# Performance work log

Hardware: AMD Instinct MI355X
Metric: run time of the kernel (lower is better)

## Reference

```python
import jax, jax.numpy as jnp
import numpy as np

B, H, W, C = 16, 64, 64, 256
NH = 8          # num_heads
WS = 8          # window size (8,8) from shift=2
HID = 1024      # mlp hidden = 4*C
EPS = 1e-5


def _rel_index():
    # relative_position_index exactly as in the torch module (meshgrid 'ij')
    ch = np.arange(WS)
    coords = np.stack(np.meshgrid(ch, ch, indexing='ij'))          # (2, WS, WS)
    flat = coords.reshape(2, -1)                                    # (2, N)
    rel = flat[:, :, None] - flat[:, None, :]                       # (2, N, N)
    rel = rel.transpose(1, 2, 0).astype(np.int64)                   # (N, N, 2)
    rel[..., 0] += WS - 1
    rel[..., 1] += WS - 1
    rel[..., 0] *= 2 * WS - 1
    return jnp.asarray(rel.sum(-1))                                 # (N, N)


def _ln(x, w, b):
    m = x.mean(-1, keepdims=True)
    v = jnp.mean((x - m) ** 2, axis=-1, keepdims=True)
    return (x - m) / jnp.sqrt(v + EPS) * w + b


def setup_inputs() -> dict:
    key = jax.random.key(0)
    ks = jax.random.split(key, 16)
    std = 0.02
    n_bias = (2 * WS - 1) * (2 * WS - 1)  # 225
    return {
        'x': jax.random.normal(ks[0], (B, H * W, C), jnp.float32),
        'norm1_w': jnp.ones((C,), jnp.float32),
        'norm1_b': jnp.zeros((C,), jnp.float32),
        'qkv_w': jax.random.normal(ks[1], (3 * C, C), jnp.float32) * std,
        'qkv_b': jnp.zeros((3 * C,), jnp.float32),
        'rel_bias': jax.random.normal(ks[2], (n_bias, NH), jnp.float32) * std,
        'proj_w': jax.random.normal(ks[3], (C, C), jnp.float32) * std,
        'proj_b': jnp.zeros((C,), jnp.float32),
        'norm2_w': jnp.ones((C,), jnp.float32),
        'norm2_b': jnp.zeros((C,), jnp.float32),
        'fc1_w': jax.random.normal(ks[4], (HID, C), jnp.float32) * std,
        'fc1_b': jnp.zeros((HID,), jnp.float32),
        'dw_w': jax.random.normal(ks[5], (3, 3, 1, HID), jnp.float32) * std,  # HWIO depthwise
        'dw_b': jnp.zeros((HID,), jnp.float32),
        'fc2_w': jax.random.normal(ks[6], (C, HID), jnp.float32) * std,
        'fc2_b': jnp.zeros((C,), jnp.float32),
    }


def reference(x, norm1_w, norm1_b, qkv_w, qkv_b, rel_bias, proj_w, proj_b,
              norm2_w, norm2_b, fc1_w, fc1_b, dw_w, dw_b, fc2_w, fc2_b):
    S = (H // WS) * (W // WS)   # num windows = 64
    N = WS * WS                 # tokens per window = 64
    shortcut = x
    h = _ln(x, norm1_w, norm1_b).reshape(B, H, W, C)
    # window partition -> (B, S, N, C), then permute to (B, N, S, C)
    hw = (h.reshape(B, H // WS, WS, W // WS, WS, C)
            .transpose(0, 1, 3, 2, 4, 5)
            .reshape(B, S, N, C))
    xw = hw.transpose(0, 2, 1, 3)            # (B, N, S, C)
    # qkv over flattened (N*S) tokens; heads split the S*C feature dim
    xf = xw.reshape(B, N * S, C)
    qkv = xf @ qkv_w.T + qkv_b               # (B, N*S, 3C)
    qkv = qkv.reshape(B, N, 3, NH, S * C // NH).transpose(2, 0, 3, 1, 4)
    q, k, v = qkv[0], qkv[1], qkv[2]         # (B, NH, N, S*C/NH)
    scale = (C // NH) ** -0.5
    attn = jnp.einsum('bhnd,bhmd->bhnm', q, k) * scale   # (B, NH, N, N)
    idx = _rel_index()
    bias = rel_bias[idx.reshape(-1)].reshape(N, N, NH).transpose(2, 0, 1)
    attn = jax.nn.softmax(attn + bias[None], axis=-1)
    out = jnp.einsum('bhnm,bhmd->bhnd', attn, v)         # (B, NH, N, S*C/NH)
    out = out.transpose(0, 2, 1, 3).reshape(B, N * S, C)
    out = (out @ proj_w.T + proj_b).reshape(B, N, S, C).transpose(0, 2, 1, 3)  # (B,S,N,C)
    # window reverse -> (B, H*W, C)
    xr = (out.reshape(B, H // WS, W // WS, WS, WS, C)
             .transpose(0, 1, 3, 2, 4, 5)
             .reshape(B, H * W, C))
    x = shortcut + xr
    # conv-based MLP (eval mode, dropout = identity)
    y = _ln(x, norm2_w, norm2_b).reshape(B, H, H, C)      # NHWC
    y = jnp.einsum('bhwc,oc->bhwo', y, fc1_w) + fc1_b     # 1x1 conv
    y = jax.lax.conv_general_dilated(
        y, dw_w, (1, 1), 'SAME',
        dimension_numbers=('NHWC', 'HWIO', 'NHWC'),
        feature_group_count=HID) + dw_b
    y = jax.nn.gelu(y, approximate=False)
    y = jnp.einsum('bhwo,co->bhwc', y, fc2_w) + fc2_b     # 1x1 conv
    return x + y.reshape(B, H * W, C)
```

## Files before the change

### kernel.cpp

```cpp
#include <hip/hip_runtime.h>
#include <hip/hip_bf16.h>
#include <cstdint>
#include <cstddef>

#define B_     16
#define HW_    4096
#define C_     256
#define NH_    8
#define S_     64
#define N_     64
#define C3_    768
#define HID_   1024
#define DHEAD_ 2048
#define EPS_   1e-5f

using u16 = unsigned short;
using u32 = unsigned int;

typedef __attribute__((ext_vector_type(8))) short bf16x8;
typedef __attribute__((ext_vector_type(4))) float f32x4;

__device__ __forceinline__ float bf2f(u16 u) {
  union { float f; u32 i; } x; x.i = ((u32)u) << 16; return x.f;
}
__device__ __forceinline__ u16 f2bf(float f) {
  union { float f; u32 i; } x; x.f = f;
  u32 r = (x.i + 0x7FFFu + ((x.i >> 16) & 1u)) >> 16;
  return (u16)r;
}

__device__ __forceinline__ void gload_lds16(const u16* g, u16* l) {
  __builtin_amdgcn_global_load_lds(
      (const __attribute__((address_space(1))) unsigned int*)g,
      (__attribute__((address_space(3))) unsigned int*)l, 16, 0, 0);
}

__launch_bounds__(256)
__global__ void pack_w_kernel(const float* __restrict__ W, u16* __restrict__ out,
                              int K, int kshift) {
  int g = blockIdx.x * 256 + threadIdx.x;
  int lane = g & 63;
  int pk = g >> 6;
  int cb = pk >> kshift;
  int kb = pk & ((1 << kshift) - 1);
  int j = cb * 16 + (lane & 15);
  int k = kb * 32 + ((lane >> 4) << 3);
  const float* src = W + (size_t)j * K + k;
  float4 a = ((const float4*)src)[0];
  float4 b = ((const float4*)src)[1];
  ushort4 lo = {f2bf(a.x), f2bf(a.y), f2bf(a.z), f2bf(a.w)};
  ushort4 hi = {f2bf(b.x), f2bf(b.y), f2bf(b.z), f2bf(b.w)};
  ushort4* dst = (ushort4*)(out + (size_t)g * 8);
  dst[0] = lo;
  dst[1] = hi;
}

__launch_bounds__(256)
__global__ void ln_kernel(const float* __restrict__ in, const float* __restrict__ w,
                          const float* __restrict__ bias, u16* __restrict__ out,
                          int b_base) {
  int wave = threadIdx.x >> 6;
  int lane = threadIdx.x & 63;
  int t = blockIdx.x * 4 + wave;
  int b = b_base + (t >> 12);
  int r = t & 4095;
  int n = r >> 6, s = r & 63;
  int hw = (((s >> 3) << 3) + (n >> 3)) * 64 + ((s & 7) << 3) + (n & 7);
  size_t src_row = ((size_t)b << 12) + hw;
  float4 v = ((const float4*)(in + src_row * C_))[lane];
  float sum = v.x + v.y + v.z + v.w;
#pragma unroll
  for (int off = 32; off; off >>= 1) sum += __shfl_xor(sum, off);
  float mean = sum * (1.0f / C_);
  float4 d = {v.x - mean, v.y - mean, v.z - mean, v.w - mean};
  float ss = d.x * d.x + d.y * d.y + d.z * d.z + d.w * d.w;
#pragma unroll
  for (int off = 32; off; off >>= 1) ss += __shfl_xor(ss, off);
  float rstd = rsqrtf(ss * (1.0f / C_) + EPS_);
  float4 w4 = ((const float4*)w)[lane];
  float4 b4 = ((const float4*)bias)[lane];
  ushort4 o;
  o.x = f2bf(d.x * rstd * w4.x + b4.x);
  o.y = f2bf(d.y * rstd * w4.y + b4.y);
  o.z = f2bf(d.z * rstd * w4.z + b4.z);
  o.w = f2bf(d.w * rstd * w4.w + b4.w);
  ((ushort4*)(out + (size_t)t * C_))[lane] = o;
}

template<int K_, int J_, int EPI>
__launch_bounds__(256)
__global__ void gemm_mfma(const u16* __restrict__ A, const u16* __restrict__ wpk,
                          const float* __restrict__ bias, u16* __restrict__ outB,
                          float* __restrict__ outF, const float* __restrict__ res,
                          int m_base, u16* __restrict__ qb, u16* __restrict__ kb,
                          u16* __restrict__ vt) {
  constexpr int NT = K_ / 64;
  __shared__ u16 As[2][128 * 64];
  int tid = threadIdx.x;
  int wid = tid >> 6, lane = tid & 63;
  int nx = gridDim.x;
  int bid = blockIdx.y * nx + blockIdx.x;
  int cpx = (nx * gridDim.y) >> 3;
  int swz = (bid & 7) * cpx + (bid >> 3);
  int n0 = (swz % nx) * 128;
  int m0 = (swz / nx) * 128;
  int wr = wid >> 1, wc = wid & 1;
  f32x4 acc[4][4] = {};
  int srow8 = lane >> 3, sslot = lane & 7;

#define ASTAGE(buf, t)                                                         \
  {                                                                            \
    int k0g = (t) * 64;                                                        \
    int cbb = ((sslot ^ srow8) << 4);                                          \
    _Pragma("unroll")                                                          \
    for (int r = 0; r < 4; ++r) {                                              \
      int row = wid * 32 + r * 8 + srow8;                                      \
      gload_lds16(A + (size_t)(m0 + row) * K_ + k0g + (cbb >> 1),              \
                  &As[buf][(wid * 32 + r * 8) * 64]);                          \
    }                                                                          \
  }

  ASTAGE(0, 0);
  asm volatile("s_waitcnt vmcnt(0)" ::: "memory");
  __builtin_amdgcn_sched_barrier(0);
  __builtin_amdgcn_s_barrier();
  __builtin_amdgcn_sched_barrier(0);

  for (int t = 0; t < NT; ++t) {
    bf16x8 bfr[8];
#pragma unroll
    for (int kk = 0; kk < 2; ++kk)
#pragma unroll
      for (int nf = 0; nf < 4; ++nf)
        bfr[kk * 4 + nf] = *(const bf16x8*)&wpk[
            ((size_t)(((n0 >> 4) + wc * 4 + nf) * (K_ / 32) + (t * 2 + kk)) * 64 + lane) * 8];
    if (t + 1 < NT) ASTAGE((t + 1) & 1, t + 1);
    const u16* as = As[t & 1];
#pragma unroll
    for (int kk = 0; kk < 2; ++kk) {
      bf16x8 afr[4];
#pragma unroll
      for (int mf = 0; mf < 4; ++mf) {
        int ra = wr * 64 + mf * 16 + (lane & 15);
        int cbb = (((kk * 4 + (lane >> 4)) ^ (ra & 7)) << 4);
        afr[mf] = *(const bf16x8*)&as[ra * 64 + (cbb >> 1)];
      }
#pragma unroll
      for (int mf = 0; mf < 4; ++mf)
#pragma unroll
        for (int nf = 0; nf < 4; ++nf)
          acc[mf][nf] = __builtin_amdgcn_mfma_f32_16x16x32_bf16(afr[mf], bfr[kk * 4 + nf], acc[mf][nf], 0, 0, 0);
    }
    asm volatile("s_waitcnt vmcnt(0)" ::: "memory");
    __builtin_amdgcn_sched_barrier(0);
    __builtin_amdgcn_s_barrier();
    __builtin_amdgcn_sched_barrier(0);
  }
#undef ASTAGE

#pragma unroll
  for (int nf = 0; nf < 4; ++nf) {
    int col = n0 + wc * 64 + nf * 16 + (lane & 15);
    float bv = bias[col];
#pragma unroll
    for (int mf = 0; mf < 4; ++mf) {
#pragma unroll
      for (int j = 0; j < 4; ++j) {
        int m = m0 + wr * 64 + mf * 16 + (lane >> 4) * 4 + j;
        float v = acc[mf][nf][j] + bv;
        if (EPI == 0) {
          outB[(size_t)m * J_ + col] = f2bf(v);
        } else if (EPI == 2) {
          size_t o = (size_t)(m_base + m) * C_ + col;
          outF[o] += v;
        } else {
          int b_rel = m >> 12, nn = (m >> 6) & 63, s = m & 63;
          int f = s * 768 + col;
          int part = f >> 14, hh = (f >> 11) & 7, d = f & 2047;
          u16 val = f2bf(v);
          size_t bh = (size_t)b_rel * 8 + hh;
          if (part == 0)      qb[(bh * 64 + nn) * 2048 + d] = val;
          else if (part == 1) kb[(bh * 64 + nn) * 2048 + d] = val;
          else                vt[(bh * 2048 + d) * 64 + nn] = val;
        }
      }
    }
  }
}

__launch_bounds__(256)
__global__ void proj_ln_fused(const u16* __restrict__ A, const u16* __restrict__ wpk,
                              const float* __restrict__ bias, const float* __restrict__ res,
                              float* __restrict__ outF, const float* __restrict__ ln_w,
                              const float* __restrict__ ln_b, u16* __restrict__ h2,
                              int m_base) {
  __shared__ u16 As[2][64 * 64];
  __shared__ float red[64][8];
  int tid = threadIdx.x;
  int wid = tid >> 6, lane = tid & 63;
  int m0 = blockIdx.x * 64;
  f32x4 acc[4][4] = {};
  int srow8 = lane >> 3, sslot = lane & 7;

#define PSTAGE(buf, t)                                                         \
  {                                                                            \
    int k0g = (t) * 64;                                                        \
    int cbb = ((sslot ^ srow8) << 4);                                          \
    _Pragma("unroll")                                                          \
    for (int r = 0; r < 2; ++r) {                                              \
      int row = wid * 16 + r * 8 + srow8;                                      \
      gload_lds16(A + (size_t)(m0 + row) * 256 + k0g + (cbb >> 1),             \
                  &As[buf][(wid * 16 + r * 8) * 64]);                          \
    }                                                                          \
  }

  PSTAGE(0, 0);
  asm volatile("s_waitcnt vmcnt(0)" ::: "memory");
  __builtin_amdgcn_sched_barrier(0);
  __builtin_amdgcn_s_barrier();
  __builtin_amdgcn_sched_barrier(0);

#pragma unroll
  for (int t = 0; t < 4; ++t) {
    bf16x8 bfr[8];
#pragma unroll
    for (int kk = 0; kk < 2; ++kk)
#pragma unroll
      for (int nf = 0; nf < 4; ++nf)
        bfr[kk * 4 + nf] = *(const bf16x8*)&wpk[
            ((size_t)((wid * 4 + nf) * 8 + (t * 2 + kk)) * 64 + lane) * 8];
    if (t + 1 < 4) PSTAGE((t + 1) & 1, t + 1);
    const u16* as = As[t & 1];
#pragma unroll
    for (int kk = 0; kk < 2; ++kk) {
      bf16x8 afr[4];
#pragma unroll
      for (int mf = 0; mf < 4; ++mf) {
        int ra = mf * 16 + (lane & 15);
        int cbb = (((kk * 4 + (lane >> 4)) ^ (ra & 7)) << 4);
        afr[mf] = *(const bf16x8*)&as[ra * 64 + (cbb >> 1)];
      }
#pragma unroll
      for (int mf = 0; mf < 4; ++mf)
#pragma unroll
        for (int nf = 0; nf < 4; ++nf)
          acc[mf][nf] = __builtin_amdgcn_mfma_f32_16x16x32_bf16(afr[mf], bfr[kk * 4 + nf], acc[mf][nf], 0, 0, 0);
    }
    asm volatile("s_waitcnt vmcnt(0)" ::: "memory");
    __builtin_amdgcn_sched_barrier(0);
    __builtin_amdgcn_s_barrier();
    __builtin_amdgcn_sched_barrier(0);
  }
#undef PSTAGE

#pragma unroll
  for (int mf = 0; mf < 4; ++mf) {
#pragma unroll
    for (int j = 0; j < 4; ++j) {
      int m = m0 + mf * 16 + (lane >> 4) * 4 + j;
      int gm = m_base + m;
      int b = gm >> 12, nn = (gm >> 6) & 63, s = gm & 63;
      int hw = (((s >> 3) << 3) + (nn >> 3)) * 64 + ((s & 7) << 3) + (nn & 7);
      size_t rowo = (((size_t)b << 12) + hw) * C_;
      float s1 = 0.f, s2 = 0.f;
#pragma unroll
      for (int nf = 0; nf < 4; ++nf) {
        int col = wid * 64 + nf * 16 + (lane & 15);
        float v = acc[mf][nf][j] + bias[col] + res[rowo + col];
        acc[mf][nf][j] = v;
        outF[rowo + col] = v;
        s1 += v; s2 += v * v;
      }
#pragma unroll
      for (int off = 1; off < 16; off <<= 1) {
        s1 += __shfl_xor(s1, off);
        s2 += __shfl_xor(s2, off);
      }
      if ((lane & 15) == 0) {
        int rr = mf * 16 + (lane >> 4) * 4 + j;
        red[rr][wid * 2] = s1;
        red[rr][wid * 2 + 1] = s2;
      }
    }
  }
  __syncthreads();

#pragma unroll
  for (int mf = 0; mf < 4; ++mf) {
#pragma unroll
    for (int j = 0; j < 4; ++j) {
      int rr = mf * 16 + (lane >> 4) * 4 + j;
      float sum = red[rr][0] + red[rr][2] + red[rr][4] + red[rr][6];
      float ssq = red[rr][1] + red[rr][3] + red[rr][5] + red[rr][7];
      float mean = sum * (1.0f / C_);
      float var = ssq * (1.0f / C_) - mean * mean;
      float rstd = rsqrtf(var + EPS_);
      int m = m0 + rr;
      int b_rel = m >> 12, nn = (m >> 6) & 63, s = m & 63;
      int hw = (((s >> 3) << 3) + (nn >> 3)) * 64 + ((s & 7) << 3) + (nn & 7);
      size_t ho = (((size_t)b_rel << 12) + hw) * C_;
#pragma unroll
      for (int nf = 0; nf < 4; ++nf) {
        int col = wid * 64 + nf * 16 + (lane & 15);
        float nv = (acc[mf][nf][j] - mean) * rstd * ln_w[col] + ln_b[col];
        h2[ho + col] = f2bf(nv);
      }
    }
  }
}

__launch_bounds__(256)
__global__ void attn_mfma(const u16* __restrict__ qb, const u16* __restrict__ kb,
                          const u16* __restrict__ vt, const float* __restrict__ rel_bias,
                          u16* __restrict__ outp) {
  __shared__ u16 bufA[4096];
  __shared__ u16 bufB[4096];
  int bid = blockIdx.x;
  int half = bid & 1;
  int bh = bid >> 1;
  int h = bh & 7;
  int b_rel = bh >> 3;
  int tid = threadIdx.x;
  int w = tid >> 6, lane = tid & 63;
  int l3 = lane >> 3, l7 = lane & 7;
  const u16* qg = qb + (size_t)bh * 64 * 2048;
  const u16* kg = kb + (size_t)bh * 64 * 2048;
  const u16* vg = vt + (size_t)bh * 2048 * 64;

  f32x4 acc[4] = {};
  for (int k0 = 0; k0 < 2048; k0 += 64) {
#pragma unroll
    for (int r = 0; r < 2; ++r) {
      int row = w * 16 + r * 8 + l3;
      int sc = (l7 ^ (row & 7)) * 8;
      gload_lds16(qg + (size_t)row * 2048 + k0 + sc, &bufA[(w * 16 + r * 8) * 64]);
      gload_lds16(kg + (size_t)row * 2048 + k0 + sc, &bufB[(w * 16 + r * 8) * 64]);
    }
    __syncthreads();
    int rowq = w * 16 + (lane & 15);
#pragma unroll
    for (int ks = 0; ks < 2; ++ks) {
      bf16x8 aq = *(const bf16x8*)&bufA[rowq * 64 + (((ks * 4 + (lane >> 4)) ^ (rowq & 7)) << 3)];
#pragma unroll
      for (int cf = 0; cf < 4; ++cf) {
        int m = cf * 16 + (lane & 15);
        bf16x8 bk = *(const bf16x8*)&bufB[m * 64 + (((ks * 4 + (lane >> 4)) ^ (m & 7)) << 3)];
        acc[cf] = __builtin_amdgcn_mfma_f32_16x16x32_bf16(aq, bk, acc[cf], 0, 0, 0);
      }
    }
    __syncthreads();
  }

  const float scale = 0.17677669529663688f;
#pragma unroll
  for (int j = 0; j < 4; ++j) {
    int r = w * 16 + (lane >> 4) * 4 + j;
    int i1 = r >> 3, j1 = r & 7;
    float v[4];
#pragma unroll
    for (int cf = 0; cf < 4; ++cf) {
      int c = cf * 16 + (lane & 15);
      int idx = (i1 - (c >> 3) + 7) * 15 + (j1 - (c & 7) + 7);
      v[cf] = acc[cf][j] * scale + rel_bias[idx * NH_ + h];
    }
    float mx = fmaxf(fmaxf(v[0], v[1]), fmaxf(v[2], v[3]));
#pragma unroll
    for (int off = 8; off; off >>= 1) mx = fmaxf(mx, __shfl_xor(mx, off));
    float sm = 0.f;
#pragma unroll
    for (int cf = 0; cf < 4; ++cf) { v[cf] = __expf(v[cf] - mx); sm += v[cf]; }
#pragma unroll
    for (int off = 8; off; off >>= 1) sm += __shfl_xor(sm, off);
    float inv = 1.0f / sm;
#pragma unroll
    for (int cf = 0; cf < 4; ++cf) {
      int c = cf * 16 + (lane & 15);
      bufA[r * 64 + (c ^ ((r & 7) << 3))] = f2bf(v[cf] * inv);
    }
  }
  __syncthreads();

  bf16x8 pa[2];
  {
    int n = w * 16 + (lane & 15);
#pragma unroll
    for (int ks = 0; ks < 2; ++ks)
      pa[ks] = *(const bf16x8*)&bufA[n * 64 + ((ks * 32 + (lane >> 4) * 8) ^ ((n & 7) << 3))];
  }

  int d0beg = half * 1024;
  for (int d0 = d0beg; d0 < d0beg + 1024; d0 += 64) {
#pragma unroll
    for (int r = 0; r < 2; ++r) {
      int drow = w * 16 + r * 8 + l3;
      int sc = (l7 ^ (drow & 7)) * 8;
      gload_lds16(vg + (size_t)(d0 + drow) * 64 + sc, &bufB[(w * 16 + r * 8) * 64]);
    }
    __syncthreads();
    f32x4 o[4] = {};
#pragma unroll
    for (int ks = 0; ks < 2; ++ks)
#pragma unroll
      for (int cf = 0; cf < 4; ++cf) {
        int d = cf * 16 + (lane & 15);
        bf16x8 bv = *(const bf16x8*)&bufB[d * 64 + (((ks * 4 + (lane >> 4)) ^ (d & 7)) << 3)];
        o[cf] = __builtin_amdgcn_mfma_f32_16x16x32_bf16(pa[ks], bv, o[cf], 0, 0, 0);
      }
#pragma unroll
    for (int cf = 0; cf < 4; ++cf) {
      int f = h * 2048 + d0 + cf * 16 + (lane & 15);
      int s = f >> 8, c = f & 255;
#pragma unroll
      for (int j = 0; j < 4; ++j) {
        int n = w * 16 + (lane >> 4) * 4 + j;
        outp[(((size_t)b_rel * 64 + n) * 64 + s) * 256 + c] = f2bf(o[cf][j]);
      }
    }
    __syncthreads();
  }
}

__launch_bounds__(256)
__global__ void dwconv_gelu(const u16* __restrict__ y1, const float* __restrict__ dw_w,
                            const float* __restrict__ dw_b, u16* __restrict__ y2) {
  int bid = blockIdx.x;
  int wt = bid & 31, ht = (bid >> 5) & 15, b = bid >> 9;
  int h0 = ht * 4, w0 = wt * 2;
  int c0 = threadIdx.x * 4;

  float4 wv[9];
#pragma unroll
  for (int i = 0; i < 9; ++i) wv[i] = *(const float4*)&dw_w[i * HID_ + c0];

  ushort4 in[6][4];
#pragma unroll
  for (int ii = 0; ii < 6; ++ii) {
    int hh = h0 + ii - 1;
#pragma unroll
    for (int jj = 0; jj < 4; ++jj) {
      int ww = w0 + jj - 1;
      if ((unsigned)hh < 64u && (unsigned)ww < 64u)
        in[ii][jj] = *(const ushort4*)(y1 + ((size_t)((b << 12) + hh * 64 + ww)) * HID_ + c0);
      else
        in[ii][jj] = ushort4{0, 0, 0, 0};
    }
  }

  float4 bv = *(const float4*)&dw_b[c0];
  float4 acc[4][2];
#pragma unroll
  for (int i = 0; i < 4; ++i)
#pragma unroll
    for (int j = 0; j < 2; ++j) acc[i][j] = bv;

#pragma unroll
  for (int ii = 0; ii < 6; ++ii) {
#pragma unroll
    for (int jj = 0; jj < 4; ++jj) {
      ushort4 u = in[ii][jj];
      float4 f = {bf2f(u.x), bf2f(u.y), bf2f(u.z), bf2f(u.w)};
#pragma unroll
      for (int kh = 0; kh < 3; ++kh) {
        int i = ii - kh;
        if (i < 0 || i > 3) continue;
#pragma unroll
        for (int kw = 0; kw < 3; ++kw) {
          int j = jj - kw;
          if (j < 0 || j > 1) continue;
          float4 w4 = wv[kh * 3 + kw];
          acc[i][j].x += f.x * w4.x;
          acc[i][j].y += f.y * w4.y;
          acc[i][j].z += f.z * w4.z;
          acc[i][j].w += f.w * w4.w;
        }
      }
    }
  }

  const float k = 0.70710678118654752f;
#pragma unroll
  for (int i = 0; i < 4; ++i) {
#pragma unroll
    for (int j = 0; j < 2; ++j) {
      float4 a = acc[i][j];
      ushort4 o;
      o.x = f2bf(0.5f * a.x * (1.0f + erff(a.x * k)));
      o.y = f2bf(0.5f * a.y * (1.0f + erff(a.y * k)));
      o.z = f2bf(0.5f * a.z * (1.0f + erff(a.z * k)));
      o.w = f2bf(0.5f * a.w * (1.0f + erff(a.w * k)));
      *(ushort4*)(y2 + ((size_t)((b << 12) + (h0 + i) * 64 + (w0 + j))) * HID_ + c0) = o;
    }
  }
}

extern "C" void kernel_launch(void* const* d_in, const int* in_sizes, int n_in,
                              void* d_out, int out_size, void* d_ws, size_t ws_size,
                              hipStream_t stream) {
  const float* x       = (const float*)d_in[0];
  const float* norm1_w = (const float*)d_in[1];
  const float* norm1_b = (const float*)d_in[2];
  const float* qkv_w   = (const float*)d_in[3];
  const float* qkv_b   = (const float*)d_in[4];
  const float* rel_b   = (const float*)d_in[5];
  const float* proj_w  = (const float*)d_in[6];
  const float* proj_b  = (const float*)d_in[7];
  const float* norm2_w = (const float*)d_in[8];
  const float* norm2_b = (const float*)d_in[9];
  const float* fc1_w   = (const float*)d_in[10];
  const float* fc1_b   = (const float*)d_in[11];
  const float* dw_w    = (const float*)d_in[12];
  const float* dw_b    = (const float*)d_in[13];
  const float* fc2_w   = (const float*)d_in[14];
  const float* fc2_b   = (const float*)d_in[15];
  float* out = (float*)d_out;
  char* ws = (char*)d_ws;

  u16* wq = (u16*)(ws);
  u16* wp = wq + 768 * 256;
  u16* w1 = wp + 256 * 256;
  u16* w2 = w1 + 1024 * 256;
  pack_w_kernel<<<768 * 256 / 8 / 256, 256, 0, stream>>>(qkv_w, wq, 256, 3);
  pack_w_kernel<<<256 * 256 / 8 / 256, 256, 0, stream>>>(proj_w, wp, 256, 3);
  pack_w_kernel<<<1024 * 256 / 8 / 256, 256, 0, stream>>>(fc1_w, w1, 256, 3);
  pack_w_kernel<<<256 * 1024 / 8 / 256, 256, 0, stream>>>(fc2_w, w2, 1024, 5);

  const size_t MBy = (size_t)1 << 20;
  char* cws = ws + 2 * MBy;
  int G = 1;
  for (int g = 16; g >= 1; g >>= 1) {
    if (2 * MBy + (size_t)(18 * g) * MBy <= ws_size) { G = g; break; }
  }
  const size_t gm = (size_t)G * MBy;
  u16* h1c    = (u16*)(cws);
  u16* qbuf   = (u16*)(cws + 2 * gm);
  u16* kbuf   = (u16*)(cws + 4 * gm);
  u16* vtbuf  = (u16*)(cws + 6 * gm);
  u16* attnoc = (u16*)(cws + 8 * gm);
  u16* h2c    = (u16*)(cws);
  u16* y1c    = (u16*)(cws + 2 * gm);
  u16* y2c    = (u16*)(cws + 10 * gm);

  const int Mloc = G * 4096;
  for (int b0 = 0; b0 < B_; b0 += G) {
    ln_kernel<<<Mloc / 4, 256, 0, stream>>>(x, norm1_w, norm1_b, h1c, b0);
    gemm_mfma<256, 768, 3><<<dim3(6, Mloc / 128), 256, 0, stream>>>(
        h1c, wq, qkv_b, nullptr, nullptr, nullptr, 0, qbuf, kbuf, vtbuf);
    attn_mfma<<<G * 16, 256, 0, stream>>>(qbuf, kbuf, vtbuf, rel_b, attnoc);
    proj_ln_fused<<<Mloc / 64, 256, 0, stream>>>(
        attnoc, wp, proj_b, x, out, norm2_w, norm2_b, h2c, b0 * 4096);
    gemm_mfma<256, 1024, 0><<<dim3(8, Mloc / 128), 256, 0, stream>>>(
        h2c, w1, fc1_b, y1c, nullptr, nullptr, 0, nullptr, nullptr, nullptr);
    dwconv_gelu<<<Mloc / 8, 256, 0, stream>>>(y1c, dw_w, dw_b, y2c);
    gemm_mfma<1024, 256, 2><<<dim3(2, Mloc / 128), 256, 0, stream>>>(
        y2c, w2, fc2_b, nullptr, out, nullptr, b0 * 4096, nullptr, nullptr, nullptr);
  }
}
```

Before: 477.2 us.

## Stage GEMM epilogues through LDS and remap block indices for XCD locality

The GEMM epilogues for the bf16 output and fp32 residual-accumulate paths now write accumulator tiles into shared memory first, then emit row-contiguous 16-byte vector stores and float4 read-modify-writes. This replaces the scattered 2-byte and 4-byte per-lane global accesses. The attention and depthwise-conv kernels also remap blockIdx so that consecutive logical blocks land on the same XCD, which aims to improve L2 reuse on the chiplet layout. The cost is extra LDS traffic and barriers in the epilogue. The remap assumes the grid size is divisible by 8.

Result: no change. 481.3 us (+0.9%).

```diff
diff --git a/kernel.cpp b/kernel.cpp
--- a/kernel.cpp
+++ b/kernel.cpp
@@ -158,22 +158,77 @@
   }
 #undef ASTAGE
 
-#pragma unroll
-  for (int nf = 0; nf < 4; ++nf) {
-    int col = n0 + wc * 64 + nf * 16 + (lane & 15);
-    float bv = bias[col];
-#pragma unroll
-    for (int mf = 0; mf < 4; ++mf) {
-#pragma unroll
-      for (int j = 0; j < 4; ++j) {
-        int m = m0 + wr * 64 + mf * 16 + (lane >> 4) * 4 + j;
-        float v = acc[mf][nf][j] + bv;
-        if (EPI == 0) {
-          outB[(size_t)m * J_ + col] = f2bf(v);
-        } else if (EPI == 2) {
-          size_t o = (size_t)(m_base + m) * C_ + col;
-          outF[o] += v;
-        } else {
+  if (EPI == 0) {
+    u16* ot = (u16*)As;
+#pragma unroll
+    for (int half = 0; half < 2; ++half) {
+      if (wr == half) {
+#pragma unroll
+        for (int nf = 0; nf < 4; ++nf) {
+          int cloc = wc * 64 + nf * 16 + (lane & 15);
+          float bv = bias[n0 + cloc];
+#pragma unroll
+          for (int mf = 0; mf < 4; ++mf)
+#pragma unroll
+            for (int j = 0; j < 4; ++j) {
+              int rloc = mf * 16 + (lane >> 4) * 4 + j;
+              ot[rloc * 136 + cloc] = f2bf(acc[mf][nf][j] + bv);
+            }
+        }
+      }
+      __syncthreads();
+#pragma unroll
+      for (int i = 0; i < 4; ++i) {
+        int c = tid + 256 * i;
+        int row = c >> 4, ch = c & 15;
+        bf16x8 v = *(const bf16x8*)&ot[row * 136 + ch * 8];
+        *(bf16x8*)&outB[(size_t)(m0 + half * 64 + row) * J_ + n0 + ch * 8] = v;
+      }
+      __syncthreads();
+    }
+  } else if (EPI == 2) {
+    float* ot32 = (float*)As;
+#pragma unroll
+    for (int q = 0; q < 4; ++q) {
+      if (wr == (q >> 1)) {
+        int mfb = (q & 1) * 2;
+#pragma unroll
+        for (int nf = 0; nf < 4; ++nf) {
+          int cloc = wc * 64 + nf * 16 + (lane & 15);
+          float bv = bias[n0 + cloc];
+#pragma unroll
+          for (int mf2 = 0; mf2 < 2; ++mf2)
+#pragma unroll
+            for (int j = 0; j < 4; ++j) {
+              int rloc = mf2 * 16 + (lane >> 4) * 4 + j;
+              ot32[rloc * 132 + cloc] = acc[mfb + mf2][nf][j] + bv;
+            }
+        }
+      }
+      __syncthreads();
+#pragma unroll
+      for (int i = 0; i < 4; ++i) {
+        int c = tid + 256 * i;
+        int row = c >> 5, ch = c & 31;
+        size_t o = (size_t)(m_base + m0 + q * 32 + row) * C_ + n0 + ch * 4;
+        float4 cur = *(const float4*)&outF[o];
+        float4 ad = *(const float4*)&ot32[row * 132 + ch * 4];
+        cur.x += ad.x; cur.y += ad.y; cur.z += ad.z; cur.w += ad.w;
+        *(float4*)&outF[o] = cur;
+      }
+      __syncthreads();
+    }
+  } else {
+#pragma unroll
+    for (int nf = 0; nf < 4; ++nf) {
+      int col = n0 + wc * 64 + nf * 16 + (lane & 15);
+      float bv = bias[col];
+#pragma unroll
+      for (int mf = 0; mf < 4; ++mf) {
+#pragma unroll
+        for (int j = 0; j < 4; ++j) {
+          int m = m0 + wr * 64 + mf * 16 + (lane >> 4) * 4 + j;
+          float v = acc[mf][nf][j] + bv;
           int b_rel = m >> 12, nn = (m >> 6) & 63, s = m & 63;
           int f = s * 768 + col;
           int part = f >> 14, hh = (f >> 11) & 7, d = f & 2047;
@@ -315,9 +370,11 @@
                           u16* __restrict__ outp) {
   __shared__ u16 bufA[4096];
   __shared__ u16 bufB[4096];
-  int bid = blockIdx.x;
-  int half = bid & 1;
-  int bh = bid >> 1;
+  int nb = gridDim.x;
+  int cpx = nb >> 3;
+  int swzb = (blockIdx.x & 7) * cpx + (blockIdx.x >> 3);
+  int half = swzb & 1;
+  int bh = swzb >> 1;
   int h = bh & 7;
   int b_rel = bh >> 3;
   int tid = threadIdx.x;
@@ -423,7 +480,9 @@
 __launch_bounds__(256)
 __global__ void dwconv_gelu(const u16* __restrict__ y1, const float* __restrict__ dw_w,
                             const float* __restrict__ dw_b, u16* __restrict__ y2) {
-  int bid = blockIdx.x;
+  int nb = gridDim.x;
+  int cpx = nb >> 3;
+  int bid = (blockIdx.x & 7) * cpx + (blockIdx.x >> 3);
   int wt = bid & 31, ht = (bid >> 5) & 15, b = bid >> 9;
   int h0 = ht * 4, w0 = wt * 2;
   int c0 = threadIdx.x * 4;
```
